# Optimization experiments

Measured on AMD Instinct MI355X. Metric: run time of the kernel, lower is better.

The kernel has to match this reference:

```python
import jax, jax.numpy as jnp
import numpy as np

B, S, D, H, DK, F = 8, 1024, 1024, 16, 64, 4096
EPS = 1e-5


def _layer_norm(x, g, b):
    mu = jnp.mean(x, axis=-1, keepdims=True)
    var = jnp.var(x, axis=-1, keepdims=True)
    return (x - mu) * jax.lax.rsqrt(var + EPS) * g + b


def setup_inputs() -> dict:
    key = jax.random.key(0)
    ks = jax.random.split(key, 16)
    s = lambda fan: 1.0 / np.sqrt(fan)
    return {
        "src": jax.random.normal(ks[0], (B, S, D), dtype=jnp.float32),
        "Wq": jax.random.uniform(ks[1], (H, D, DK), jnp.float32, -s(D), s(D)),
        "bq": jnp.zeros((H, DK), jnp.float32),
        "Wk": jax.random.uniform(ks[2], (H, D, DK), jnp.float32, -s(D), s(D)),
        "bk": jnp.zeros((H, DK), jnp.float32),
        "Wv": jax.random.uniform(ks[3], (H, D, DK), jnp.float32, -s(D), s(D)),
        "bv": jnp.zeros((H, DK), jnp.float32),
        "Wo": jax.random.uniform(ks[4], (H * DK, D), jnp.float32, -s(H * DK), s(H * DK)),
        "bo": jnp.zeros((D,), jnp.float32),
        "g1": jnp.ones((D,), jnp.float32),
        "be1": jnp.zeros((D,), jnp.float32),
        "W1": jax.random.uniform(ks[5], (D, F), jnp.float32, -s(D), s(D)),
        "b1": jnp.zeros((F,), jnp.float32),
        "W2": jax.random.uniform(ks[6], (F, D), jnp.float32, -s(F), s(F)),
        "b2": jnp.zeros((D,), jnp.float32),
        "g2": jnp.ones((D,), jnp.float32),
        "be2": jnp.zeros((D,), jnp.float32),
    }


def reference(src, Wq, bq, Wk, bk, Wv, bv, Wo, bo, g1, be1, W1, b1, W2, b2, g2, be2):
    # Per-head projections (vectorized over the Python head loop of the original)
    q = jnp.einsum("bsd,hdk->bhsk", src, Wq) + bq[:, None, :]
    k = jnp.einsum("bsd,hdk->bhsk", src, Wk) + bk[:, None, :]
    v = jnp.einsum("bsd,hdk->bhsk", src, Wv) + bv[:, None, :]
    scale = 1.0 / jnp.sqrt(jnp.asarray(DK, src.dtype))
    scores = jnp.einsum("bhsk,bhtk->bhst", q, k) * scale  # [B,H,S,S]
    attn = jax.nn.softmax(scores, axis=-1)
    o = jnp.einsum("bhst,bhtk->bhsk", attn, v)
    # torch.cat over heads on last dim -> [B,S,H*DK] with head-major feature order
    o = o.transpose(0, 2, 1, 3).reshape(B, S, H * DK)
    attn_out = o @ Wo + bo
    x = _layer_norm(src + attn_out, g1, be1)  # dropout inactive at inference
    ff = jax.nn.relu(x @ W1 + b1) @ W2 + b2
    return _layer_norm(x + ff, g2, be2)
```

## Files before the change

### kernel.cpp

```cpp
#include <hip/hip_runtime.h>

#define Bq 8
#define Sq 1024
#define Dq 1024
#define Hq 16
#define DKq 64
#define Fq 4096
#define TOK (Bq*Sq)

typedef unsigned short u16;
typedef unsigned int u32;
typedef __bf16 bf16x8 __attribute__((ext_vector_type(8)));
typedef float  f32x4  __attribute__((ext_vector_type(4)));

__device__ __forceinline__ float bf2f(u16 u) {
  u32 x = ((u32)u) << 16;
  float f; __builtin_memcpy(&f, &x, 4); return f;
}
__device__ __forceinline__ u16 f2bf(float f) {
  u32 u; __builtin_memcpy(&u, &f, 4);
  u += 0x7fffu + ((u >> 16) & 1u);
  return (u16)(u >> 16);
}
__device__ __forceinline__ void async16(const u16* g, u16* l) {
  __builtin_amdgcn_global_load_lds(
      (__attribute__((address_space(1))) void*)(g),
      (__attribute__((address_space(3))) void*)(l), 16, 0, 0);
}
__device__ __forceinline__ u16 load_in(const void* p, long idx, u32 fp32) {
  return fp32 ? f2bf(((const float*)p)[idx]) : ((const u16*)p)[idx];
}
__device__ __forceinline__ int swzb(int row, int colb) {
  return row * 128 + (colb ^ ((row & 7) << 4));
}

struct InTab { const void* p[17]; int n[17]; };

__global__ void detect_all(InTab tab, u32* flags) {
  __shared__ int sh[3][256];
  int bi = blockIdx.x;
  const u16* buf = (const u16*)tab.p[bi];
  long n = tab.n[bi];
  long m = n < 65536 ? n : 65536;
  int t = threadIdx.x;
  int nanpat = 0, evz = 0, oddnz = 0;
  for (long i = t; i < m; i += 256) {
    u16 v = buf[i];
    if ((v & 0x7F80u) == 0x7F80u) nanpat++;
    if ((i & 1) == 0) { if (v == 0) evz++; }
    else { if (v != 0) oddnz++; }
  }
  sh[0][t] = nanpat; sh[1][t] = evz; sh[2][t] = oddnz;
  __syncthreads();
  for (int s = 128; s > 0; s >>= 1) {
    if (t < s) { sh[0][t] += sh[0][t+s]; sh[1][t] += sh[1][t+s]; sh[2][t] += sh[2][t+s]; }
    __syncthreads();
  }
  if (t == 0) {
    long half = m / 2;
    bool fp32 = (sh[0][0] > 8) ||
                (sh[1][0] > (half * 9) / 10 && sh[2][0] > (half * 9) / 10);
    flags[bi] = fp32 ? 1u : 0u;
  }
}

__global__ void diag_ws_too_small(u16* out, float code) { out[0] = f2bf(code); }

__global__ void diag_mixed(const u32* flags, void* out) {
  u32 a = flags[0];
  if (flags[1] != a || flags[7] != a || flags[11] != a || flags[13] != a) {
    if (a) ((float*)out)[0] = 3000.0f;
    else ((u16*)out)[0] = f2bf(3000.0f);
  }
}

__global__ __launch_bounds__(256) void pack_all(const void* __restrict__ Wq,
                                                const void* __restrict__ Wk,
                                                const void* __restrict__ Wv,
                                                const void* __restrict__ Wo,
                                                const void* __restrict__ W1,
                                                const void* __restrict__ W2,
                                                u16* __restrict__ Wqkv_t,
                                                u16* __restrict__ Wo_t,
                                                u16* __restrict__ W1_t,
                                                u16* __restrict__ W2_t,
                                                const u32* __restrict__ flags) {
  int id = blockIdx.x;
  const void* in; u16* out; u32 f; int R, C; long zin; int r0, c0;
  if (id < 768) {
    int w = id >> 8, t = id & 255;
    int z = t >> 4, xt = t & 15;
    in = (w == 0) ? Wq : ((w == 1) ? Wk : Wv);
    f = flags[(w == 0) ? 1 : ((w == 1) ? 3 : 5)];
    R = 1024; C = 64;
    zin = (long)z * 65536;
    out = Wqkv_t + (long)w * 1048576 + (long)z * 65536;
    r0 = xt * 64; c0 = 0;
  } else if (id < 1024) {
    int t = id - 768; int xt = t & 15, yt = t >> 4;
    in = Wo; f = flags[7]; R = 1024; C = 1024; zin = 0; out = Wo_t;
    r0 = xt * 64; c0 = yt * 64;
  } else if (id < 2048) {
    int t = id - 1024; int xt = t & 15, yt = t >> 4;
    in = W1; f = flags[11]; R = 1024; C = 4096; zin = 0; out = W1_t;
    r0 = xt * 64; c0 = yt * 64;
  } else {
    int t = id - 2048; int xt = t & 63, yt = t >> 6;
    in = W2; f = flags[13]; R = 4096; C = 1024; zin = 0; out = W2_t;
    r0 = xt * 64; c0 = yt * 64;
  }
  __shared__ u16 tile[64][65];
  int tx = threadIdx.x & 63, ty = threadIdx.x >> 6;
#pragma unroll
  for (int it = 0; it < 16; it++) {
    int row = it * 4 + ty;
    tile[row][tx] = load_in(in, zin + (long)(r0 + row) * C + (c0 + tx), f);
  }
  __syncthreads();
#pragma unroll
  for (int it = 0; it < 16; it++) {
    int cc = it * 4 + ty;
    out[(long)(c0 + cc) * R + r0 + tx] = tile[tx][cc];
  }
}

struct CvtTab { const void* p[10]; int flagidx[10]; int dstoff[10]; int n[10]; };
__global__ void cvt_small(CvtTab tab, u16* __restrict__ dst, const u32* __restrict__ flags) {
  int e = blockIdx.x;
  u32 f = flags[tab.flagidx[e]];
  const void* p = tab.p[e];
  int n = tab.n[e], o = tab.dstoff[e];
  for (int i = threadIdx.x; i < n; i += 256) dst[o + i] = load_in(p, i, f);
}

__global__ __launch_bounds__(256) void cvt_src(const void* __restrict__ in,
                                               u16* __restrict__ out,
                                               const u32* __restrict__ flag) {
  u32 f = *flag;
  long i8 = ((long)blockIdx.x * 256 + threadIdx.x) * 8;
  if (f) {
    const float4* f4 = (const float4*)((const float*)in + i8);
    float4 a = f4[0], b = f4[1];
    u16 v[8] = {f2bf(a.x), f2bf(a.y), f2bf(a.z), f2bf(a.w),
                f2bf(b.x), f2bf(b.y), f2bf(b.z), f2bf(b.w)};
    *(uint4*)(out + i8) = *(const uint4*)v;
  } else {
    *(uint4*)(out + i8) = *(const uint4*)((const u16*)in + i8);
  }
}

__global__ __launch_bounds__(256) void gemm_bt(const u16* __restrict__ A,
                                               const u16* __restrict__ Bt,
                                               const u16* __restrict__ bias,
                                               u16* __restrict__ C,
                                               int M, int N, int K, int act) {
  __shared__ alignas(16) u16 sA[2][128 * 32];
  __shared__ alignas(16) u16 sB[2][128 * 32];
  const int tid = threadIdx.x;
  const int wv = tid >> 6, lane = tid & 63;
  const int m16 = lane & 15, quad = lane >> 4;
  const long bm = (long)blockIdx.x * 128;
  const long bn = (long)blockIdx.y * 128;
  const int wm = (wv >> 1) * 64, wn = (wv & 1) * 64;

  f32x4 acc[4][4];
#pragma unroll
  for (int i = 0; i < 4; i++)
#pragma unroll
    for (int j = 0; j < 4; j++) acc[i][j] = (f32x4){0.f, 0.f, 0.f, 0.f};

  const int row_s = tid >> 2;
  const int col_s = (tid & 3) * 8;
  const u16* gA0 = A + (bm + row_s) * (long)K + col_s;
  const u16* gA1 = gA0 + 64 * (long)K;
  const u16* gB0 = Bt + (bn + row_s) * (long)K + col_s;
  const u16* gB1 = gB0 + 64 * (long)K;

  auto stage = [&](int p, int k) {
    async16(gA0 + k, &sA[p][wv * 512]);
    async16(gA1 + k, &sA[p][2048 + wv * 512]);
    async16(gB0 + k, &sB[p][wv * 512]);
    async16(gB1 + k, &sB[p][2048 + wv * 512]);
  };
  auto compute = [&](int p) {
    bf16x8 af[4], bf_[4];
#pragma unroll
    for (int mi = 0; mi < 4; mi++)
      af[mi] = *(const bf16x8*)&sA[p][(wm + mi * 16 + m16) * 32 + quad * 8];
#pragma unroll
    for (int ni = 0; ni < 4; ni++)
      bf_[ni] = *(const bf16x8*)&sB[p][(wn + ni * 16 + m16) * 32 + quad * 8];
#pragma unroll
    for (int mi = 0; mi < 4; mi++)
#pragma unroll
      for (int ni = 0; ni < 4; ni++)
        acc[mi][ni] = __builtin_amdgcn_mfma_f32_16x16x32_bf16(af[mi], bf_[ni], acc[mi][ni], 0, 0, 0);
  };

  stage(0, 0);
  for (int k0 = 0; k0 < K; k0 += 64) {
    __syncthreads();
    if (k0 + 32 < K) stage(1, k0 + 32);
    compute(0);
    __syncthreads();
    if (k0 + 64 < K) stage(0, k0 + 64);
    compute(1);
  }

  float bv4[4];
#pragma unroll
  for (int ni = 0; ni < 4; ni++) bv4[ni] = bf2f(bias[bn + wn + ni * 16 + m16]);

#pragma unroll
  for (int mi = 0; mi < 4; mi++) {
#pragma unroll
    for (int ni = 0; ni < 4; ni++) {
      long col = bn + wn + ni * 16 + m16;
#pragma unroll
      for (int r = 0; r < 4; r++) {
        long row = bm + wm + mi * 16 + quad * 4 + r;
        float v = acc[mi][ni][r] + bv4[ni];
        if (act) v = fmaxf(v, 0.f);
        C[row * N + col] = f2bf(v);
      }
    }
  }
}

#define MF16 __builtin_amdgcn_mfma_f32_16x16x32_bf16

#define TILE256(BUF, NBUF, DOA, DOB, KA, KB, VMS)                              \
  {                                                                            \
                   \
    _Pragma("unroll") for (int mi = 0; mi < 4; mi++)                           \
      _Pragma("unroll") for (int kk = 0; kk < 2; kk++)                         \
        afr[mi][kk] = *(const bf16x8*)&sA[BUF][offA + mi * 1024 + kof[kk]];    \
    _Pragma("unroll") for (int ni = 0; ni < 2; ni++)                           \
      _Pragma("unroll") for (int kk = 0; kk < 2; kk++)                         \
        bfr[ni][kk] = *(const bf16x8*)&sB[BUF][offB + ni * 1024 + kof[kk]];    \
    if (DOA) stA(NBUF, 0, KA);                                                 \
    __builtin_amdgcn_s_barrier();                                              \
    __builtin_amdgcn_s_setprio(1);                                             \
    _Pragma("unroll") for (int kk = 0; kk < 2; kk++)                           \
      _Pragma("unroll") for (int mi = 0; mi < 4; mi++)                         \
        _Pragma("unroll") for (int ni = 0; ni < 2; ni++)                       \
          acc[mi][ni] = MF16(afr[mi][kk], bfr[ni][kk], acc[mi][ni], 0, 0, 0);  \
    __builtin_amdgcn_s_setprio(0);                                             \
    __builtin_amdgcn_s_barrier();                                              \
                                 \
    _Pragma("unroll") for (int ni = 0; ni < 2; ni++)                           \
      _Pragma("unroll") for (int kk = 0; kk < 2; kk++)                         \
        bfr[2 + ni][kk] = *(const bf16x8*)&sB[BUF][offB + (2 + ni) * 1024 + kof[kk]]; \
    if (DOA) stA(NBUF, 1, KA);                                                 \
    __builtin_amdgcn_s_barrier();                                              \
    __builtin_amdgcn_s_setprio(1);                                             \
    _Pragma("unroll") for (int kk = 0; kk < 2; kk++)                           \
      _Pragma("unroll") for (int mi = 0; mi < 4; mi++)                         \
        _Pragma("unroll") for (int ni = 0; ni < 2; ni++)                       \
          acc[mi][2 + ni] = MF16(afr[mi][kk], bfr[2 + ni][kk], acc[mi][2 + ni], 0, 0, 0); \
    __builtin_amdgcn_s_setprio(0);                                             \
    __builtin_amdgcn_s_barrier();                                              \
     \
    _Pragma("unroll") for (int mi = 0; mi < 4; mi++)                           \
      _Pragma("unroll") for (int kk = 0; kk < 2; kk++)                         \
        afr[mi][kk] = *(const bf16x8*)&sA[BUF][offA + (4 + mi) * 1024 + kof[kk]]; \
    if (DOB) stB(BUF, 0, KB);                                                  \
    __builtin_amdgcn_s_barrier();                                              \
    __builtin_amdgcn_s_setprio(1);                                             \
    _Pragma("unroll") for (int kk = 0; kk < 2; kk++)                           \
      _Pragma("unroll") for (int mi = 0; mi < 4; mi++)                         \
        _Pragma("unroll") for (int ni = 0; ni < 2; ni++)                       \
          acc[4 + mi][2 + ni] = MF16(afr[mi][kk], bfr[2 + ni][kk], acc[4 + mi][2 + ni], 0, 0, 0); \
    __builtin_amdgcn_s_setprio(0);                                             \
    __builtin_amdgcn_s_barrier();                                              \
           \
    if (DOB) stB(BUF, 1, KB);                                                  \
    asm volatile("s_waitcnt vmcnt(" VMS ")" ::: "memory");                     \
    __builtin_amdgcn_s_barrier();                                              \
    __builtin_amdgcn_s_setprio(1);                                             \
    _Pragma("unroll") for (int kk = 0; kk < 2; kk++)                           \
      _Pragma("unroll") for (int mi = 0; mi < 4; mi++)                         \
        _Pragma("unroll") for (int ni = 0; ni < 2; ni++)                       \
          acc[4 + mi][ni] = MF16(afr[mi][kk], bfr[ni][kk], acc[4 + mi][ni], 0, 0, 0); \
    __builtin_amdgcn_s_setprio(0);                                             \
    __builtin_amdgcn_s_barrier();                                              \
  }

__global__ __launch_bounds__(512, 2) void gemm256(const u16* __restrict__ A,
                                                  const u16* __restrict__ Bt,
                                                  const u16* __restrict__ bias,
                                                  u16* __restrict__ C,
                                                  int M, int N, int K, int act,
                                                  int ldc, u16* __restrict__ Vt,
                                                  int mode) {
  __shared__ alignas(16) u16 sA[2][16384];
  __shared__ alignas(16) u16 sB[2][16384];
  const int tid = threadIdx.x;
  const int wv = tid >> 6, lane = tid & 63;
  const int m16 = lane & 15, quad = lane >> 4;
  const int wr = wv >> 2, wc = wv & 3;

  const int NT = N >> 8;
  int bid = blockIdx.x;
  {
    const int nwg = gridDim.x;
    const int q = nwg >> 3, r = nwg & 7;
    const int xcd = bid & 7, lp = bid >> 3;
    bid = (xcd < r ? xcd * (q + 1) : r * (q + 1) + (xcd - r) * q) + lp;
  }
  const long bm = (long)(bid / NT) * 256;
  const long bn = (long)(bid % NT) * 256;

  const int r0 = wv * 16 + (lane >> 3);
  const int cstg = ((lane & 7) ^ (lane >> 3)) * 8;
  const u16* gA0 = A  + (bm + r0) * (long)K + cstg;
  const u16* gA1 = A  + (bm + 128 + r0) * (long)K + cstg;
  const u16* gB0 = Bt + (bn + r0) * (long)K + cstg;
  const u16* gB1 = Bt + (bn + 128 + r0) * (long)K + cstg;
  const long k8 = 8 * (long)K;

  auto stA = [&](int nb, int h, int k0) {
    const u16* s = (h ? gA1 : gA0) + k0;
    u16* d = &sA[nb][h * 8192 + wv * 1024];
    async16(s, d);
    async16(s + k8, d + 512);
  };
  auto stB = [&](int nb, int h, int k0) {
    const u16* s = (h ? gB1 : gB0) + k0;
    u16* d = &sB[nb][h * 8192 + wv * 1024];
    async16(s, d);
    async16(s + k8, d + 512);
  };

  const int qs = quad ^ (m16 & 3);
  const int hb = (m16 >> 2) & 1;
  const int kof[2] = {hb * 32, 32 - hb * 32};
  const int offA = wr * 8192 + m16 * 64 + qs * 8;
  const int offB = (wc >> 1) * 8192 + (wc & 1) * 4096 + m16 * 64 + qs * 8;

  f32x4 acc[8][4];
#pragma unroll
  for (int i = 0; i < 8; i++)
#pragma unroll
    for (int j = 0; j < 4; j++) acc[i][j] = (f32x4){0.f, 0.f, 0.f, 0.f};
  bf16x8 afr[4][2], bfr[4][2];

  const int KT = K >> 6;

  stA(0, 0, 0); stA(0, 1, 0); stB(0, 0, 0); stB(0, 1, 0);
  stB(1, 0, 64); stB(1, 1, 64);
  asm volatile("s_waitcnt vmcnt(4)" ::: "memory");
  __builtin_amdgcn_s_barrier();

  int T = 0;
  for (; T + 2 < KT; T += 2) {
    const int kA1 = (T + 1) << 6, kB2 = (T + 2) << 6, kB3 = (T + 3) << 6;
    TILE256(0, 1, true, true, kA1, kB2, "4");
    TILE256(1, 0, true, true, kB2, kB3, "4");
  }
  {
    const int kA1 = (T + 1) << 6;
    TILE256(0, 1, true, false, kA1, 0, "0");
    TILE256(1, 0, false, false, 0, 0, "0");
  }

  float bv4[4];
#pragma unroll
  for (int ni = 0; ni < 4; ni++) bv4[ni] = bf2f(bias[bn + wc * 64 + ni * 16 + m16]);

#pragma unroll
  for (int mi = 0; mi < 8; mi++) {
#pragma unroll
    for (int ni = 0; ni < 4; ni++) {
      long col = bn + wc * 64 + ni * 16 + m16;
      long rowb = bm + wr * 128 + mi * 16 + quad * 4;
      if (mode == 1 && col >= 2048) {
        int hh = ((int)col >> 6) & 15, dk = (int)col & 63;
        int bb = (int)(rowb >> 10), ss = (int)(rowb & 1023);
        u16 t4[4];
#pragma unroll
        for (int r = 0; r < 4; r++) t4[r] = f2bf(acc[mi][ni][r] + bv4[ni]);
        *(uint2*)&Vt[(((long)bb * 16 + hh) * 64 + dk) * 1024 + ss] = *(const uint2*)t4;
      } else {
#pragma unroll
        for (int r = 0; r < 4; r++) {
          float v = acc[mi][ni][r] + bv4[ni];
          if (act) v = fmaxf(v, 0.f);
          C[(rowb + r) * (long)ldc + col] = f2bf(v);
        }
      }
    }
  }
}

#define TILE128(BUF, NBUF, DOA, DOB, KA, KB, VMS)                              \
  {                                                                            \
                           \
    _Pragma("unroll") for (int mi = 0; mi < 4; mi++)                           \
      _Pragma("unroll") for (int kk = 0; kk < 2; kk++)                         \
        afr[mi][kk] = *(const bf16x8*)&sA[BUF][offA + mi * 1024 + kof[kk]];    \
    _Pragma("unroll") for (int ni = 0; ni < 2; ni++)                           \
      _Pragma("unroll") for (int kk = 0; kk < 2; kk++)                         \
        bfr[ni][kk] = *(const bf16x8*)&sB[BUF][offB + ni * 1024 + kof[kk]];    \
    if (DOA) stA(NBUF, 0, KA);                                                 \
    __builtin_amdgcn_s_barrier();                                              \
    __builtin_amdgcn_s_setprio(1);                                             \
    _Pragma("unroll") for (int kk = 0; kk < 2; kk++)                           \
      _Pragma("unroll") for (int mi = 0; mi < 4; mi++)                         \
        _Pragma("unroll") for (int ni = 0; ni < 2; ni++)                       \
          acc[mi][ni] = MF16(afr[mi][kk], bfr[ni][kk], acc[mi][ni], 0, 0, 0);  \
    __builtin_amdgcn_s_setprio(0);                                             \
    __builtin_amdgcn_s_barrier();                                              \
                            \
    _Pragma("unroll") for (int ni = 0; ni < 2; ni++)                           \
      _Pragma("unroll") for (int kk = 0; kk < 2; kk++)                         \
        bfr[2 + ni][kk] = *(const bf16x8*)&sB[BUF][offB + (2 + ni) * 1024 + kof[kk]]; \
    if (DOA) stA(NBUF, 1, KA);                                                 \
    __builtin_amdgcn_s_barrier();                                              \
    __builtin_amdgcn_s_setprio(1);                                             \
    _Pragma("unroll") for (int kk = 0; kk < 2; kk++)                           \
      _Pragma("unroll") for (int mi = 0; mi < 4; mi++)                         \
        _Pragma("unroll") for (int ni = 0; ni < 2; ni++)                       \
          acc[mi][2 + ni] = MF16(afr[mi][kk], bfr[2 + ni][kk], acc[mi][2 + ni], 0, 0, 0); \
    __builtin_amdgcn_s_setprio(0);                                             \
    __builtin_amdgcn_s_barrier();                                              \
                   \
    if (DOB) stB(BUF, KB);                                                     \
    asm volatile("s_waitcnt vmcnt(" VMS ")" ::: "memory");                     \
    __builtin_amdgcn_s_barrier();                                              \
  }

__global__ __launch_bounds__(512, 2) void gemm256x128(const u16* __restrict__ A,
                                                      const u16* __restrict__ Bt,
                                                      const u16* __restrict__ bias,
                                                      u16* __restrict__ C,
                                                      int M, int N, int K, int act) {
  __shared__ alignas(16) u16 sA[2][16384];
  __shared__ alignas(16) u16 sB[2][8192];
  const int tid = threadIdx.x;
  const int wv = tid >> 6, lane = tid & 63;
  const int m16 = lane & 15, quad = lane >> 4;
  const int wr = wv >> 1, wc = wv & 1;

  const int NT = N >> 7;
  int bid = blockIdx.x;
  {
    const int nwg = gridDim.x;
    const int q = nwg >> 3, r = nwg & 7;
    const int xcd = bid & 7, lp = bid >> 3;
    bid = (xcd < r ? xcd * (q + 1) : r * (q + 1) + (xcd - r) * q) + lp;
  }
  const long bm = (long)(bid / NT) * 256;
  const long bn = (long)(bid % NT) * 128;

  const int r0 = wv * 16 + (lane >> 3);
  const int cstg = ((lane & 7) ^ (lane >> 3)) * 8;
  const u16* gA0 = A + (bm + r0) * (long)K + cstg;
  const u16* gA1 = A + (bm + 128 + r0) * (long)K + cstg;
  const u16* gB0 = Bt + (bn + r0) * (long)K + cstg;
  const long k8 = 8 * (long)K;

  auto stA = [&](int nb, int h, int k0) {
    const u16* s = (h ? gA1 : gA0) + k0;
    u16* d = &sA[nb][h * 8192 + wv * 1024];
    async16(s, d);
    async16(s + k8, d + 512);
  };
  auto stB = [&](int nb, int k0) {
    const u16* s = gB0 + k0;
    u16* d = &sB[nb][wv * 1024];
    async16(s, d);
    async16(s + k8, d + 512);
  };

  const int qs = quad ^ (m16 & 3);
  const int hb = (m16 >> 2) & 1;
  const int kof[2] = {hb * 32, 32 - hb * 32};
  const int offA = (wr >> 1) * 8192 + (wr & 1) * 4096 + m16 * 64 + qs * 8;
  const int offB = wc * 4096 + m16 * 64 + qs * 8;

  f32x4 acc[4][4];
#pragma unroll
  for (int i = 0; i < 4; i++)
#pragma unroll
    for (int j = 0; j < 4; j++) acc[i][j] = (f32x4){0.f, 0.f, 0.f, 0.f};
  bf16x8 afr[4][2], bfr[4][2];

  const int KT = K >> 6;

  stA(0, 0, 0); stA(0, 1, 0); stB(0, 0);
  stB(1, 64);
  asm volatile("s_waitcnt vmcnt(2)" ::: "memory");
  __builtin_amdgcn_s_barrier();

  int T = 0;
  for (; T + 2 < KT; T += 2) {
    TILE128(0, 1, true, true, (T + 1) << 6, (T + 2) << 6, "2");
    TILE128(1, 0, true, true, (T + 2) << 6, (T + 3) << 6, "2");
  }
  TILE128(0, 1, true, false, (T + 1) << 6, 0, "0");
  TILE128(1, 0, false, false, 0, 0, "0");

  float bv4[4];
#pragma unroll
  for (int ni = 0; ni < 4; ni++) bv4[ni] = bf2f(bias[bn + wc * 64 + ni * 16 + m16]);

#pragma unroll
  for (int mi = 0; mi < 4; mi++) {
#pragma unroll
    for (int ni = 0; ni < 4; ni++) {
      long col = bn + wc * 64 + ni * 16 + m16;
      long rowb = bm + wr * 64 + mi * 16 + quad * 4;
#pragma unroll
      for (int r = 0; r < 4; r++) {
        float v = acc[mi][ni][r] + bv4[ni];
        if (act) v = fmaxf(v, 0.f);
        C[(rowb + r) * (long)N + col] = f2bf(v);
      }
    }
  }
}

__global__ __launch_bounds__(256, 4) void attn_fwd(const u16* __restrict__ qk,
                                                   const u16* __restrict__ Vt,
                                                   u16* __restrict__ attnO) {
  __shared__ alignas(16) u16 sQP[8192];
  __shared__ alignas(16) u16 sK[4096];
  __shared__ alignas(16) u16 sVt[4096];
  const int tid = threadIdx.x;
  const int bh = blockIdx.x;
  const int qt = blockIdx.y;
  const int b = bh >> 4, h = bh & 15;
  const int wv = tid >> 6, lane = tid & 63;
  const int m16 = lane & 15, quad = lane >> 4;
  const int kk = tid >> 3;
  const int t7 = tid & 7;

  char* cQP = (char*)sQP;
  char* cK = (char*)sK;
  char* cV = (char*)sVt;

  {
    int row = tid >> 1, half = tid & 1;
    const u16* g = qk + (long)(b * Sq + qt * 128 + row) * 2048 + h * 64 + half * 32;
#pragma unroll
    for (int j = 0; j < 4; j++) {
      uint4 raw = *(const uint4*)(g + j * 8);
      const u16* pv = (const u16*)&raw;
      u16 t[8];
#pragma unroll
      for (int e = 0; e < 8; e++) t[e] = f2bf(bf2f(pv[e]) * 0.125f);
      *(uint4*)(cQP + swzb(row, half * 64 + j * 16)) = *(const uint4*)t;
    }
  }
  __syncthreads();
  bf16x8 qf[2][2];
#pragma unroll
  for (int qt2 = 0; qt2 < 2; qt2++)
#pragma unroll
    for (int s = 0; s < 2; s++)
      qf[qt2][s] = *(const bf16x8*)(cQP + swzb(wv * 32 + qt2 * 16 + m16, s * 64 + quad * 16));

  f32x4 o[4][2];
#pragma unroll
  for (int dt = 0; dt < 4; dt++)
#pragma unroll
    for (int qt2 = 0; qt2 < 2; qt2++) o[dt][qt2] = (f32x4){0.f, 0.f, 0.f, 0.f};
  float mrun[2] = {-1e30f, -1e30f}, lrun[2] = {0.f, 0.f};

  const u16* gK = qk + (long)(b * Sq + kk) * 2048 + 1024 + h * 64 + t7 * 8;
  const u16* gV = Vt + ((long)bh * 64 + kk) * 1024 + t7 * 8;
  const long stepK = (long)64 * 2048;
  const int off0 = swzb(kk, t7 * 16);
  const int off1 = off0 + 4096;

  uint4 rk0 = *(const uint4*)gK;
  uint4 rk1 = *(const uint4*)(gK + 32 * 2048);
  uint4 rv0 = *(const uint4*)gV;
  uint4 rv1 = *(const uint4*)(gV + 32 * 1024);

  for (int kt = 0; kt < 16; kt++) {
    __syncthreads();
    *(uint4*)(cK + off0) = rk0;
    *(uint4*)(cK + off1) = rk1;
    *(uint4*)(cV + off0) = rv0;
    *(uint4*)(cV + off1) = rv1;
    __syncthreads();

    f32x4 st[4][2];
#pragma unroll
    for (int kt2 = 0; kt2 < 4; kt2++)
#pragma unroll
      for (int qt2 = 0; qt2 < 2; qt2++) st[kt2][qt2] = (f32x4){0.f, 0.f, 0.f, 0.f};
    __builtin_amdgcn_s_setprio(1);
#pragma unroll
    for (int s = 0; s < 2; s++) {
      bf16x8 kf[4];
#pragma unroll
      for (int kt2 = 0; kt2 < 4; kt2++)
        kf[kt2] = *(const bf16x8*)(cK + swzb(kt2 * 16 + m16, s * 64 + quad * 16));
#pragma unroll
      for (int kt2 = 0; kt2 < 4; kt2++)
#pragma unroll
        for (int qt2 = 0; qt2 < 2; qt2++)
          st[kt2][qt2] = MF16(kf[kt2], qf[qt2][s], st[kt2][qt2], 0, 0, 0);
    }
    __builtin_amdgcn_s_setprio(0);

    if (kt < 15) {
      rk0 = *(const uint4*)(gK + (long)(kt + 1) * stepK);
      rk1 = *(const uint4*)(gK + (long)(kt + 1) * stepK + 32 * 2048);
      rv0 = *(const uint4*)(gV + (kt + 1) * 64);
      rv1 = *(const uint4*)(gV + (kt + 1) * 64 + 32 * 1024);
    }

    char* cP = cQP + wv * 4096;
#pragma unroll
    for (int qt2 = 0; qt2 < 2; qt2++) {
      float pm = st[0][qt2][0];
#pragma unroll
      for (int kt2 = 0; kt2 < 4; kt2++)
#pragma unroll
        for (int r = 0; r < 4; r++) pm = fmaxf(pm, st[kt2][qt2][r]);
      pm = fmaxf(pm, __shfl_xor(pm, 16));
      pm = fmaxf(pm, __shfl_xor(pm, 32));
      float mnew = fmaxf(mrun[qt2], pm);
      float al = __expf(mrun[qt2] - mnew);
      mrun[qt2] = mnew;
      float rs = 0.f;
#pragma unroll
      for (int kt2 = 0; kt2 < 4; kt2++) {
        u16 t4[4];
#pragma unroll
        for (int r = 0; r < 4; r++) {
          float p = __expf(st[kt2][qt2][r] - mnew);
          rs += p;
          t4[r] = f2bf(p);
        }
        *(uint2*)(cP + swzb(qt2 * 16 + m16, kt2 * 32 + quad * 8)) = *(const uint2*)t4;
      }
      rs += __shfl_xor(rs, 16);
      rs += __shfl_xor(rs, 32);
      lrun[qt2] = lrun[qt2] * al + rs;
#pragma unroll
      for (int dt = 0; dt < 4; dt++)
#pragma unroll
        for (int r = 0; r < 4; r++) o[dt][qt2][r] *= al;
    }

    bf16x8 pb[2][2];
#pragma unroll
    for (int qt2 = 0; qt2 < 2; qt2++)
#pragma unroll
      for (int ks = 0; ks < 2; ks++)
        pb[qt2][ks] = *(const bf16x8*)(cP + swzb(qt2 * 16 + m16, ks * 64 + quad * 16));
    __builtin_amdgcn_s_setprio(1);
#pragma unroll
    for (int dt = 0; dt < 4; dt++) {
      bf16x8 v0 = *(const bf16x8*)(cV + swzb(dt * 16 + m16, quad * 16));
      bf16x8 v1 = *(const bf16x8*)(cV + swzb(dt * 16 + m16, 64 + quad * 16));
#pragma unroll
      for (int qt2 = 0; qt2 < 2; qt2++) {
        o[dt][qt2] = MF16(v0, pb[qt2][0], o[dt][qt2], 0, 0, 0);
        o[dt][qt2] = MF16(v1, pb[qt2][1], o[dt][qt2], 0, 0, 0);
      }
    }
    __builtin_amdgcn_s_setprio(0);
  }

#pragma unroll
  for (int qt2 = 0; qt2 < 2; qt2++) {
    float rl = 1.f / lrun[qt2];
    long tok = (long)(b * Sq + qt * 128 + wv * 32 + qt2 * 16 + m16);
#pragma unroll
    for (int dt = 0; dt < 4; dt++) {
      u16 t4[4];
#pragma unroll
      for (int r = 0; r < 4; r++) t4[r] = f2bf(o[dt][qt2][r] * rl);
      *(uint2*)&attnO[tok * 1024 + h * 64 + dt * 16 + quad * 4] = *(const uint2*)t4;
    }
  }
}

__global__ __launch_bounds__(256) void add_ln(const u16* __restrict__ X,
                                              const u16* __restrict__ Y,
                                              const u16* __restrict__ g,
                                              const u16* __restrict__ be,
                                              u16* __restrict__ out) {
  const int row = blockIdx.x;
  const int t = threadIdx.x;
  const long base = (long)row * Dq;
  float v[4]; float s = 0.f, ss = 0.f;
#pragma unroll
  for (int i = 0; i < 4; i++) {
    int idx = i * 256 + t;
    float x = bf2f(X[base + idx]) + bf2f(Y[base + idx]);
    v[i] = x; s += x; ss += x * x;
  }
#pragma unroll
  for (int off = 32; off > 0; off >>= 1) { s += __shfl_down(s, off); ss += __shfl_down(ss, off); }
  __shared__ float red[8];
  int wv = t >> 6, ln = t & 63;
  if (ln == 0) { red[wv] = s; red[4 + wv] = ss; }
  __syncthreads();
  s = red[0] + red[1] + red[2] + red[3];
  ss = red[4] + red[5] + red[6] + red[7];
  float mean = s * (1.f / Dq);
  float var = ss * (1.f / Dq) - mean * mean;
  float rstd = rsqrtf(var + 1e-5f);
#pragma unroll
  for (int i = 0; i < 4; i++) {
    int idx = i * 256 + t;
    float o = (v[i] - mean) * rstd * bf2f(g[idx]) + bf2f(be[idx]);
    out[base + idx] = f2bf(o);
  }
}

__global__ __launch_bounds__(256) void add_ln_out(const u16* __restrict__ X,
                                                  const u16* __restrict__ Y,
                                                  const u16* __restrict__ g,
                                                  const u16* __restrict__ be,
                                                  void* __restrict__ out,
                                                  const u32* __restrict__ outflag) {
  const u32 fp32 = *outflag;
  const int row = blockIdx.x;
  const int t = threadIdx.x;
  const long base = (long)row * Dq;
  float v[4]; float s = 0.f, ss = 0.f;
#pragma unroll
  for (int i = 0; i < 4; i++) {
    int idx = i * 256 + t;
    float x = bf2f(X[base + idx]) + bf2f(Y[base + idx]);
    v[i] = x; s += x; ss += x * x;
  }
#pragma unroll
  for (int off = 32; off > 0; off >>= 1) { s += __shfl_down(s, off); ss += __shfl_down(ss, off); }
  __shared__ float red[8];
  int wv = t >> 6, ln = t & 63;
  if (ln == 0) { red[wv] = s; red[4 + wv] = ss; }
  __syncthreads();
  s = red[0] + red[1] + red[2] + red[3];
  ss = red[4] + red[5] + red[6] + red[7];
  float mean = s * (1.f / Dq);
  float var = ss * (1.f / Dq) - mean * mean;
  float rstd = rsqrtf(var + 1e-5f);
#pragma unroll
  for (int i = 0; i < 4; i++) {
    int idx = i * 256 + t;
    float o = (v[i] - mean) * rstd * bf2f(g[idx]) + bf2f(be[idx]);
    if (fp32) ((float*)out)[base + idx] = o;
    else ((u16*)out)[base + idx] = f2bf(o);
  }
}

extern "C" void kernel_launch(void* const* d_in, const int* in_sizes, int n_in,
                              void* d_out, int out_size, void* d_ws, size_t ws_size,
                              hipStream_t stream) {
  char* ws = (char*)d_ws;
  size_t off = 0;
  auto alloc = [&](size_t bytes) {
    void* p = ws + off;
    off += (bytes + 255) & ~(size_t)255;
    return p;
  };
  u32* flags  = (u32*)alloc(32 * 4);
  u16* Wqkv_t = (u16*)alloc((size_t)3072 * 1024 * 2);
  u16* Wo_t   = (u16*)alloc((size_t)1024 * 1024 * 2);
  u16* W1_t   = (u16*)alloc((size_t)4096 * 1024 * 2);
  u16* W2_t   = (u16*)alloc((size_t)1024 * 4096 * 2);
  u16* svec   = (u16*)alloc((size_t)13312 * 2);
  u16* src_bf = (u16*)alloc((size_t)TOK * 1024 * 2);
  u16* regA   = (u16*)alloc((size_t)TOK * 4096 * 2);
  size_t need_chunk2 = off;
  size_t need_full   = off + (size_t)TOK * 4096 * 2 / 2;

  u16* outw = (u16*)d_out;
  int CH;
  if (ws_size >= need_full) { CH = 8192; (void)alloc((size_t)32 << 20); }
  else if (ws_size >= need_chunk2) CH = 4096;
  else if (ws_size >= need_chunk2 - ((size_t)16 << 20)) CH = 2048;
  else {
    diag_ws_too_small<<<1, 1, 0, stream>>>(outw, 8000.0f + (float)(ws_size >> 20));
    return;
  }

  u16* qk    = regA;
  u16* Vt    = regA + (size_t)TOK * 2048;
  u16* attnb = regA + (size_t)TOK * 3072;
  u16* proj  = regA;
  u16* x     = regA + (size_t)TOK * 1024;
  u16* h1    = regA + (size_t)TOK * 2048;
  u16* f2    = src_bf;

  u16* bqkv = svec + 0;
  u16* bo_c = svec + 3072;
  u16* g1_c = svec + 4096;
  u16* be1_c = svec + 5120;
  u16* b1_c = svec + 6144;
  u16* b2_c = svec + 10240;
  u16* g2_c = svec + 11264;
  u16* be2_c = svec + 12288;

  InTab itab;
  for (int i = 0; i < 17; i++) { itab.p[i] = d_in[i]; itab.n[i] = in_sizes[i]; }
  detect_all<<<dim3(17), 256, 0, stream>>>(itab, flags);

  pack_all<<<dim3(3072), 256, 0, stream>>>(d_in[1], d_in[3], d_in[5], d_in[7], d_in[11], d_in[13],
                                           Wqkv_t, Wo_t, W1_t, W2_t, flags);

  CvtTab ct;
  const int srcs[10] = {2, 4, 6, 8, 9, 10, 12, 14, 15, 16};
  const int offs[10] = {0, 1024, 2048, 3072, 4096, 5120, 6144, 10240, 11264, 12288};
  const int lens[10] = {1024, 1024, 1024, 1024, 1024, 1024, 4096, 1024, 1024, 1024};
  for (int e = 0; e < 10; e++) { ct.p[e] = d_in[srcs[e]]; ct.flagidx[e] = srcs[e]; ct.dstoff[e] = offs[e]; ct.n[e] = lens[e]; }
  cvt_small<<<dim3(10), 256, 0, stream>>>(ct, svec, flags);

  cvt_src<<<dim3(TOK * 1024 / (256 * 8)), 256, 0, stream>>>(d_in[0], src_bf, &flags[0]);

  gemm256<<<dim3(32 * 12), 512, 0, stream>>>(src_bf, Wqkv_t, bqkv, qk, TOK, 3072, 1024, 0,
                                             2048, Vt, 1);
  attn_fwd<<<dim3(128, 8), 256, 0, stream>>>(qk, Vt, attnb);
  gemm256x128<<<dim3(256), 512, 0, stream>>>(attnb, Wo_t, bo_c, proj, TOK, 1024, 1024, 0);
  add_ln<<<dim3(TOK), 256, 0, stream>>>(src_bf, proj, g1_c, be1_c, x);
  for (int c = 0; c < TOK / CH; c++) {
    const u16* xc = x + (size_t)c * CH * 1024;
    u16* f2c = f2 + (size_t)c * CH * 1024;
    if (CH >= 4096) {
      gemm256<<<dim3((CH / 256) * 16), 512, 0, stream>>>(xc, W1_t, b1_c, h1, CH, 4096, 1024, 1,
                                                         4096, nullptr, 0);
    } else {
      gemm_bt<<<dim3(CH / 128, 32), 256, 0, stream>>>(xc, W1_t, b1_c, h1, CH, 4096, 1024, 1);
    }
    if (CH == 8192) {
      gemm256x128<<<dim3((CH / 256) * 8), 512, 0, stream>>>(h1, W2_t, b2_c, f2c, CH, 1024, 4096, 0);
    } else {
      gemm_bt<<<dim3(CH / 128, 8), 256, 0, stream>>>(h1, W2_t, b2_c, f2c, CH, 1024, 4096, 0);
    }
  }
  add_ln_out<<<dim3(TOK), 256, 0, stream>>>(x, f2, g2_c, be2_c, d_out, &flags[0]);
  diag_mixed<<<1, 1, 0, stream>>>(flags, d_out);
}
```

Measured before the change: 573.0 us.

## Restructure 256-tile GEMM into two-phase wide schedule, move QKV to 128 GEMM, vectorize layernorm

```diff
diff --git a/kernel.cpp b/kernel.cpp
--- a/kernel.cpp
+++ b/kernel.cpp
@@ -153,7 +153,9 @@
                                                const u16* __restrict__ Bt,
                                                const u16* __restrict__ bias,
                                                u16* __restrict__ C,
-                                               int M, int N, int K, int act) {
+                                               int M, int N, int K, int act,
+                                               int ldc, u16* __restrict__ Vt,
+                                               int mode) {
   __shared__ alignas(16) u16 sA[2][128 * 32];
   __shared__ alignas(16) u16 sB[2][128 * 32];
   const int tid = threadIdx.x;
@@ -216,12 +218,21 @@
 #pragma unroll
     for (int ni = 0; ni < 4; ni++) {
       long col = bn + wn + ni * 16 + m16;
-#pragma unroll
-      for (int r = 0; r < 4; r++) {
-        long row = bm + wm + mi * 16 + quad * 4 + r;
-        float v = acc[mi][ni][r] + bv4[ni];
-        if (act) v = fmaxf(v, 0.f);
-        C[row * N + col] = f2bf(v);
+      long rowb = bm + wm + mi * 16 + quad * 4;
+      if (mode == 1 && col >= 2048) {
+        int hh = ((int)col >> 6) & 15, dk = (int)col & 63;
+        int bb = (int)(rowb >> 10), ss = (int)(rowb & 1023);
+        u16 t4[4];
+#pragma unroll
+        for (int r = 0; r < 4; r++) t4[r] = f2bf(acc[mi][ni][r] + bv4[ni]);
+        *(uint2*)&Vt[(((long)bb * 16 + hh) * 64 + dk) * 1024 + ss] = *(const uint2*)t4;
+      } else {
+#pragma unroll
+        for (int r = 0; r < 4; r++) {
+          float v = acc[mi][ni][r] + bv4[ni];
+          if (act) v = fmaxf(v, 0.f);
+          C[(rowb + r) * (long)ldc + col] = f2bf(v);
+        }
       }
     }
   }
@@ -229,70 +240,42 @@
 
 #define MF16 __builtin_amdgcn_mfma_f32_16x16x32_bf16
 
-#define TILE256(BUF, NBUF, DOA, DOB, KA, KB, VMS)                              \
+#define TILEW(BUF, NBUF, DOA, DOB, KA, KB, VMS)                                \
   {                                                                            \
-                   \
-    _Pragma("unroll") for (int mi = 0; mi < 4; mi++)                           \
+              \
+    _Pragma("unroll") for (int mi = 0; mi < 8; mi++)                           \
       _Pragma("unroll") for (int kk = 0; kk < 2; kk++)                         \
         afr[mi][kk] = *(const bf16x8*)&sA[BUF][offA + mi * 1024 + kof[kk]];    \
-    _Pragma("unroll") for (int ni = 0; ni < 2; ni++)                           \
+    _Pragma("unroll") for (int ni = 0; ni < 4; ni++)                           \
       _Pragma("unroll") for (int kk = 0; kk < 2; kk++)                         \
         bfr[ni][kk] = *(const bf16x8*)&sB[BUF][offB + ni * 1024 + kof[kk]];    \
-    if (DOA) stA(NBUF, 0, KA);                                                 \
+    if (DOA) { stA(NBUF, 0, KA); stA(NBUF, 1, KA); }                           \
     __builtin_amdgcn_s_barrier();                                              \
     __builtin_amdgcn_s_setprio(1);                                             \
     _Pragma("unroll") for (int kk = 0; kk < 2; kk++)                           \
-      _Pragma("unroll") for (int mi = 0; mi < 4; mi++)                         \
+      _Pragma("unroll") for (int mi = 0; mi < 8; mi++)                         \
         _Pragma("unroll") for (int ni = 0; ni < 2; ni++)                       \
           acc[mi][ni] = MF16(afr[mi][kk], bfr[ni][kk], acc[mi][ni], 0, 0, 0);  \
     __builtin_amdgcn_s_setprio(0);                                             \
     __builtin_amdgcn_s_barrier();                                              \
-                                 \
-    _Pragma("unroll") for (int ni = 0; ni < 2; ni++)                           \
-      _Pragma("unroll") for (int kk = 0; kk < 2; kk++)                         \
-        bfr[2 + ni][kk] = *(const bf16x8*)&sB[BUF][offB + (2 + ni) * 1024 + kof[kk]]; \
-    if (DOA) stA(NBUF, 1, KA);                                                 \
+     \
+    if (DOB) { stB(BUF, 0, KB); stB(BUF, 1, KB); }                             \
+    asm volatile("s_waitcnt vmcnt(" VMS ")" ::: "memory");                     \
     __builtin_amdgcn_s_barrier();                                              \
     __builtin_amdgcn_s_setprio(1);                                             \
     _Pragma("unroll") for (int kk = 0; kk < 2; kk++)                           \
-      _Pragma("unroll") for (int mi = 0; mi < 4; mi++)                         \
+      _Pragma("unroll") for (int mi = 0; mi < 8; mi++)                         \
         _Pragma("unroll") for (int ni = 0; ni < 2; ni++)                       \
           acc[mi][2 + ni] = MF16(afr[mi][kk], bfr[2 + ni][kk], acc[mi][2 + ni], 0, 0, 0); \
     __builtin_amdgcn_s_setprio(0);                                             \
     __builtin_amdgcn_s_barrier();                                              \
-     \
-    _Pragma("unroll") for (int mi = 0; mi < 4; mi++)                           \
-      _Pragma("unroll") for (int kk = 0; kk < 2; kk++)                         \
-        afr[mi][kk] = *(const bf16x8*)&sA[BUF][offA + (4 + mi) * 1024 + kof[kk]]; \
-    if (DOB) stB(BUF, 0, KB);                                                  \
-    __builtin_amdgcn_s_barrier();                                              \
-    __builtin_amdgcn_s_setprio(1);                                             \
-    _Pragma("unroll") for (int kk = 0; kk < 2; kk++)                           \
-      _Pragma("unroll") for (int mi = 0; mi < 4; mi++)                         \
-        _Pragma("unroll") for (int ni = 0; ni < 2; ni++)                       \
-          acc[4 + mi][2 + ni] = MF16(afr[mi][kk], bfr[2 + ni][kk], acc[4 + mi][2 + ni], 0, 0, 0); \
-    __builtin_amdgcn_s_setprio(0);                                             \
-    __builtin_amdgcn_s_barrier();                                              \
-           \
-    if (DOB) stB(BUF, 1, KB);                                                  \
-    asm volatile("s_waitcnt vmcnt(" VMS ")" ::: "memory");                     \
-    __builtin_amdgcn_s_barrier();                                              \
-    __builtin_amdgcn_s_setprio(1);                                             \
-    _Pragma("unroll") for (int kk = 0; kk < 2; kk++)                           \
-      _Pragma("unroll") for (int mi = 0; mi < 4; mi++)                         \
-        _Pragma("unroll") for (int ni = 0; ni < 2; ni++)                       \
-          acc[4 + mi][ni] = MF16(afr[mi][kk], bfr[ni][kk], acc[4 + mi][ni], 0, 0, 0); \
-    __builtin_amdgcn_s_setprio(0);                                             \
-    __builtin_amdgcn_s_barrier();                                              \
-  }
-
-__global__ __launch_bounds__(512, 2) void gemm256(const u16* __restrict__ A,
-                                                  const u16* __restrict__ Bt,
-                                                  const u16* __restrict__ bias,
-                                                  u16* __restrict__ C,
-                                                  int M, int N, int K, int act,
-                                                  int ldc, u16* __restrict__ Vt,
-                                                  int mode) {
+  }
+
+__global__ __launch_bounds__(512, 2) void gemm256w(const u16* __restrict__ A,
+                                                   const u16* __restrict__ Bt,
+                                                   const u16* __restrict__ bias,
+                                                   u16* __restrict__ C,
+                                                   int M, int N, int K, int act) {
   __shared__ alignas(16) u16 sA[2][16384];
   __shared__ alignas(16) u16 sB[2][16384];
   const int tid = threadIdx.x;
@@ -343,7 +326,7 @@
   for (int i = 0; i < 8; i++)
 #pragma unroll
     for (int j = 0; j < 4; j++) acc[i][j] = (f32x4){0.f, 0.f, 0.f, 0.f};
-  bf16x8 afr[4][2], bfr[4][2];
+  bf16x8 afr[8][2], bfr[4][2];
 
   const int KT = K >> 6;
 
@@ -354,14 +337,12 @@
 
   int T = 0;
   for (; T + 2 < KT; T += 2) {
-    const int kA1 = (T + 1) << 6, kB2 = (T + 2) << 6, kB3 = (T + 3) << 6;
-    TILE256(0, 1, true, true, kA1, kB2, "4");
-    TILE256(1, 0, true, true, kB2, kB3, "4");
+    TILEW(0, 1, true, true, (T + 1) << 6, (T + 2) << 6, "4");
+    TILEW(1, 0, true, true, (T + 2) << 6, (T + 3) << 6, "4");
   }
   {
-    const int kA1 = (T + 1) << 6;
-    TILE256(0, 1, true, false, kA1, 0, "0");
-    TILE256(1, 0, false, false, 0, 0, "0");
+    TILEW(0, 1, true, false, (T + 1) << 6, 0, "0");
+    TILEW(1, 0, false, false, 0, 0, "0");
   }
 
   float bv4[4];
@@ -374,20 +355,11 @@
     for (int ni = 0; ni < 4; ni++) {
       long col = bn + wc * 64 + ni * 16 + m16;
       long rowb = bm + wr * 128 + mi * 16 + quad * 4;
-      if (mode == 1 && col >= 2048) {
-        int hh = ((int)col >> 6) & 15, dk = (int)col & 63;
-        int bb = (int)(rowb >> 10), ss = (int)(rowb & 1023);
-        u16 t4[4];
-#pragma unroll
-        for (int r = 0; r < 4; r++) t4[r] = f2bf(acc[mi][ni][r] + bv4[ni]);
-        *(uint2*)&Vt[(((long)bb * 16 + hh) * 64 + dk) * 1024 + ss] = *(const uint2*)t4;
-      } else {
-#pragma unroll
-        for (int r = 0; r < 4; r++) {
-          float v = acc[mi][ni][r] + bv4[ni];
-          if (act) v = fmaxf(v, 0.f);
-          C[(rowb + r) * (long)ldc + col] = f2bf(v);
-        }
+#pragma unroll
+      for (int r = 0; r < 4; r++) {
+        float v = acc[mi][ni][r] + bv4[ni];
+        if (act) v = fmaxf(v, 0.f);
+        C[(rowb + r) * (long)N + col] = f2bf(v);
       }
     }
   }
@@ -690,11 +662,15 @@
   const int row = blockIdx.x;
   const int t = threadIdx.x;
   const long base = (long)row * Dq;
+  const int i4 = t * 4;
+  uint2 xr = *(const uint2*)&X[base + i4];
+  uint2 yr = *(const uint2*)&Y[base + i4];
+  const u16* xp = (const u16*)&xr;
+  const u16* yp = (const u16*)&yr;
   float v[4]; float s = 0.f, ss = 0.f;
 #pragma unroll
   for (int i = 0; i < 4; i++) {
-    int idx = i * 256 + t;
-    float x = bf2f(X[base + idx]) + bf2f(Y[base + idx]);
+    float x = bf2f(xp[i]) + bf2f(yp[i]);
     v[i] = x; s += x; ss += x * x;
   }
 #pragma unroll
@@ -708,12 +684,15 @@
   float mean = s * (1.f / Dq);
   float var = ss * (1.f / Dq) - mean * mean;
   float rstd = rsqrtf(var + 1e-5f);
-#pragma unroll
-  for (int i = 0; i < 4; i++) {
-    int idx = i * 256 + t;
-    float o = (v[i] - mean) * rstd * bf2f(g[idx]) + bf2f(be[idx]);
-    out[base + idx] = f2bf(o);
-  }
+  uint2 gr = *(const uint2*)&g[i4];
+  uint2 br = *(const uint2*)&be[i4];
+  const u16* gp = (const u16*)&gr;
+  const u16* bp = (const u16*)&br;
+  u16 o4[4];
+#pragma unroll
+  for (int i = 0; i < 4; i++)
+    o4[i] = f2bf((v[i] - mean) * rstd * bf2f(gp[i]) + bf2f(bp[i]));
+  *(uint2*)&out[base + i4] = *(const uint2*)o4;
 }
 
 __global__ __launch_bounds__(256) void add_ln_out(const u16* __restrict__ X,
@@ -726,11 +705,15 @@
   const int row = blockIdx.x;
   const int t = threadIdx.x;
   const long base = (long)row * Dq;
+  const int i4 = t * 4;
+  uint2 xr = *(const uint2*)&X[base + i4];
+  uint2 yr = *(const uint2*)&Y[base + i4];
+  const u16* xp = (const u16*)&xr;
+  const u16* yp = (const u16*)&yr;
   float v[4]; float s = 0.f, ss = 0.f;
 #pragma unroll
   for (int i = 0; i < 4; i++) {
-    int idx = i * 256 + t;
-    float x = bf2f(X[base + idx]) + bf2f(Y[base + idx]);
+    float x = bf2f(xp[i]) + bf2f(yp[i]);
     v[i] = x; s += x; ss += x * x;
   }
 #pragma unroll
@@ -744,12 +727,23 @@
   float mean = s * (1.f / Dq);
   float var = ss * (1.f / Dq) - mean * mean;
   float rstd = rsqrtf(var + 1e-5f);
-#pragma unroll
-  for (int i = 0; i < 4; i++) {
-    int idx = i * 256 + t;
-    float o = (v[i] - mean) * rstd * bf2f(g[idx]) + bf2f(be[idx]);
-    if (fp32) ((float*)out)[base + idx] = o;
-    else ((u16*)out)[base + idx] = f2bf(o);
+  uint2 gr = *(const uint2*)&g[i4];
+  uint2 br = *(const uint2*)&be[i4];
+  const u16* gp = (const u16*)&gr;
+  const u16* bp = (const u16*)&br;
+  if (fp32) {
+    float4 o4;
+    o4.x = (v[0] - mean) * rstd * bf2f(gp[0]) + bf2f(bp[0]);
+    o4.y = (v[1] - mean) * rstd * bf2f(gp[1]) + bf2f(bp[1]);
+    o4.z = (v[2] - mean) * rstd * bf2f(gp[2]) + bf2f(bp[2]);
+    o4.w = (v[3] - mean) * rstd * bf2f(gp[3]) + bf2f(bp[3]);
+    *(float4*)((float*)out + base + i4) = o4;
+  } else {
+    u16 o4[4];
+#pragma unroll
+    for (int i = 0; i < 4; i++)
+      o4[i] = f2bf((v[i] - mean) * rstd * bf2f(gp[i]) + bf2f(bp[i]));
+    *(uint2*)((u16*)out + base + i4) = *(const uint2*)o4;
   }
 }
 
@@ -817,8 +811,8 @@
 
   cvt_src<<<dim3(TOK * 1024 / (256 * 8)), 256, 0, stream>>>(d_in[0], src_bf, &flags[0]);
 
-  gemm256<<<dim3(32 * 12), 512, 0, stream>>>(src_bf, Wqkv_t, bqkv, qk, TOK, 3072, 1024, 0,
-                                             2048, Vt, 1);
+  gemm_bt<<<dim3(64, 24), 256, 0, stream>>>(src_bf, Wqkv_t, bqkv, qk, TOK, 3072, 1024, 0,
+                                            2048, Vt, 1);
   attn_fwd<<<dim3(128, 8), 256, 0, stream>>>(qk, Vt, attnb);
   gemm256x128<<<dim3(256), 512, 0, stream>>>(attnb, Wo_t, bo_c, proj, TOK, 1024, 1024, 0);
   add_ln<<<dim3(TOK), 256, 0, stream>>>(src_bf, proj, g1_c, be1_c, x);
@@ -826,15 +820,16 @@
     const u16* xc = x + (size_t)c * CH * 1024;
     u16* f2c = f2 + (size_t)c * CH * 1024;
     if (CH >= 4096) {
-      gemm256<<<dim3((CH / 256) * 16), 512, 0, stream>>>(xc, W1_t, b1_c, h1, CH, 4096, 1024, 1,
-                                                         4096, nullptr, 0);
+      gemm256w<<<dim3((CH / 256) * 16), 512, 0, stream>>>(xc, W1_t, b1_c, h1, CH, 4096, 1024, 1);
     } else {
-      gemm_bt<<<dim3(CH / 128, 32), 256, 0, stream>>>(xc, W1_t, b1_c, h1, CH, 4096, 1024, 1);
+      gemm_bt<<<dim3(CH / 128, 32), 256, 0, stream>>>(xc, W1_t, b1_c, h1, CH, 4096, 1024, 1,
+                                                      4096, nullptr, 0);
     }
     if (CH == 8192) {
       gemm256x128<<<dim3((CH / 256) * 8), 512, 0, stream>>>(h1, W2_t, b2_c, f2c, CH, 1024, 4096, 0);
     } else {
-      gemm_bt<<<dim3(CH / 128, 8), 256, 0, stream>>>(h1, W2_t, b2_c, f2c, CH, 1024, 4096, 0);
+      gemm_bt<<<dim3(CH / 128, 8), 256, 0, stream>>>(h1, W2_t, b2_c, f2c, CH, 1024, 4096, 0,
+                                                     1024, nullptr, 0);
     }
   }
   add_ln_out<<<dim3(TOK), 256, 0, stream>>>(x, f2, g2_c, be2_c, d_out, &flags[0]);
```

Result: slower. 594.7 us (+3.8%).
